# Performance work log

Hardware: AMD Instinct MI355X
Metric: run time of the kernel (lower is better)

Reference implementation:

```python
import jax, jax.numpy as jnp
import numpy as np

OUT_F, IN_F, GROUP = 4096, 4096, 64  # meta['shape'] = (OUT_F, IN_F), group_size=64, axis=1
TOKENS = 8192  # batch*seq flattened


def dequant(W_q, scale, zero):
    # unpack_4bit_u8: high nibble = first half of rows, low nibble = second half
    hi = (W_q >> 4).astype(jnp.float32)
    lo = (W_q & 0xF).astype(jnp.float32)
    W_r = jnp.concatenate([hi, lo], axis=0)      # [G, GROUP]
    W_r = (W_r - zero) * scale                   # group-wise dequant (axis=1 grouping)
    return W_r.reshape(OUT_F, IN_F)


def setup_inputs() -> dict:
    key = jax.random.key(0)
    k0, k1, k2, k3, k4 = jax.random.split(key, 5)
    G = OUT_F * IN_F // GROUP  # 262144 groups
    x = jax.random.normal(k0, (TOKENS, IN_F), dtype=jnp.float32)
    W_q = jax.random.randint(k1, (G // 2, GROUP), 0, 256, dtype=jnp.int32)  # packed bytes
    scale = jax.random.uniform(k2, (G, 1), dtype=jnp.float32) * 0.01 + 1e-4  # 1/scale from quantizer
    zero = jax.random.uniform(k3, (G, 1), dtype=jnp.float32) * 15.0
    bias = jax.random.normal(k4, (OUT_F,), dtype=jnp.float32)
    return {"x": x, "W_q": W_q, "scale": scale, "zero": zero, "bias": bias}


def reference(x, W_q, scale, zero, bias):
    # HQQMatmulNoCacheDeq.forward: out = x @ dequantize().T + bias
    W_r = dequant(W_q, scale, zero)              # [OUT_F, IN_F]
    return x @ W_r.T + bias                      # [TOKENS, OUT_F]
```

## Files before the change

### kernel.cpp

```cpp
#include <hip/hip_runtime.h>
#include <stdint.h>


typedef __attribute__((ext_vector_type(8))) _Float16 half8;
typedef __attribute__((ext_vector_type(4))) float f32x4;

#define M_DIM 8192
#define N_DIM 4096
#define K_DIM 4096

__device__ __forceinline__ void async16(const void* g, void* l) {
  __builtin_amdgcn_global_load_lds(
      (const __attribute__((address_space(1))) void*)g,
      (__attribute__((address_space(3))) void*)l,
      16, 0, 0);
}

__global__ __launch_bounds__(256) void prep(
    const float* __restrict__ x, const int* __restrict__ Wq,
    const float* __restrict__ scale, const float* __restrict__ zero,
    _Float16* __restrict__ xh, _Float16* __restrict__ wh) {
  const int b = blockIdx.x;
  if (b < 16384) {
    const size_t i = ((size_t)b * 256 + threadIdx.x) * 8;
    f32x4 a = *(const f32x4*)(x + i);
    f32x4 c = *(const f32x4*)(x + i + 4);
    half8 h;
    h[0] = (_Float16)a[0]; h[1] = (_Float16)a[1];
    h[2] = (_Float16)a[2]; h[3] = (_Float16)a[3];
    h[4] = (_Float16)c[0]; h[5] = (_Float16)c[1];
    h[6] = (_Float16)c[2]; h[7] = (_Float16)c[3];
    *(half8*)(xh + i) = h;
  } else {
    const int idx = (b - 16384) * 256 + threadIdx.x;
    const int o  = idx >> 9;
    const int kb = (idx & 511) << 3;
    const int g  = (o << 6) + (kb >> 6);
    const int j  = kb & 63;
    const bool hi = (o < 2048);
    const int* src = Wq + (size_t)(hi ? g : g - 131072) * 64 + j;
    const int4 v0 = *(const int4*)src;
    const int4 v1 = *(const int4*)(src + 4);
    const float s  = scale[g];
    const float nz = -zero[g] * s;
    int raw[8] = {v0.x, v0.y, v0.z, v0.w, v1.x, v1.y, v1.z, v1.w};
    half8 h;
#pragma unroll
    for (int r = 0; r < 8; ++r) {
      const int nib = hi ? ((raw[r] >> 4) & 0xF) : (raw[r] & 0xF);
      h[r] = (_Float16)((float)nib * s + nz);
    }
    *(half8*)(wh + (size_t)o * K_DIM + kb) = h;
  }
}

__global__ __launch_bounds__(512, 2) void gemm_f16_deep(
    const _Float16* __restrict__ A, const _Float16* __restrict__ B,
    const float* __restrict__ bias, float* __restrict__ C) {
  __shared__ _Float16 As[3 * 8192];
  __shared__ _Float16 Bs[3 * 8192];

  const int tid  = threadIdx.x;
  const int wave = tid >> 6;
  const int lane = tid & 63;
  const int quad = lane >> 4;
  const int l16  = lane & 15;
  const int wm   = wave >> 2;
  const int wn   = wave & 3;

  const int bid = blockIdx.x;
  const int swb = (bid & 7) * 64 + (bid >> 3);
  const int m0 = (swb >> 4) * 256;
  const int n0 = (swb & 15) * 256;

  const int srow = tid >> 2;
  const int sg   = (((tid & 3) ^ ((srow >> 1) & 3)) << 3);
  const _Float16* gA0 = A + (size_t)(m0 + srow) * K_DIM + sg;
  const _Float16* gA1 = gA0 + (size_t)128 * K_DIM;
  const _Float16* gB0 = B + (size_t)(n0 + srow) * K_DIM + sg;
  const _Float16* gB1 = gB0 + (size_t)128 * K_DIM;
  const int wst = wave * 512;

  const int fro  = ((quad ^ ((l16 >> 1) & 3)) << 3);
  const int arow = wm * 128 + l16;
  const int brow = wn * 64 + l16;

  f32x4 acc[8][4] = {};

  int sR = 0, sN = 8192, sW = 16384;

  async16(gA0,      As + sR + wst);
  async16(gA1,      As + sR + 4096 + wst);
  async16(gB0,      Bs + sR + wst);
  async16(gB1,      Bs + sR + 4096 + wst);
  async16(gA0 + 32, As + sN + wst);
  async16(gA1 + 32, As + sN + 4096 + wst);
  async16(gB0 + 32, Bs + sN + wst);
  async16(gB1 + 32, Bs + sN + 4096 + wst);
  asm volatile("s_waitcnt vmcnt(4)" ::: "memory");
  __builtin_amdgcn_s_barrier();

  const int NT = K_DIM / 32;
#pragma unroll 1
  for (int T = 0; T < NT; ++T) {
    if (T + 2 < NT) {
      const int kk = (T + 2) * 32;
      async16(gA0 + kk, As + sW + wst);
      async16(gA1 + kk, As + sW + 4096 + wst);
      async16(gB0 + kk, Bs + sW + wst);
      async16(gB1 + kk, Bs + sW + 4096 + wst);
    }

    const _Float16* Ab = As + sR;
    const _Float16* Bb = Bs + sR;
    half8 aF[4], bF[4];
#pragma unroll
    for (int j = 0; j < 4; ++j)
      bF[j] = *(const half8*)(Bb + (brow + j * 16) * 32 + fro);
#pragma unroll
    for (int i = 0; i < 4; ++i)
      aF[i] = *(const half8*)(Ab + (arow + i * 16) * 32 + fro);

    __builtin_amdgcn_s_setprio(1);
#pragma unroll
    for (int i = 0; i < 4; ++i)
#pragma unroll
      for (int j = 0; j < 4; ++j)
        acc[i][j] = __builtin_amdgcn_mfma_f32_16x16x32_f16(aF[i], bF[j],
                                                           acc[i][j], 0, 0, 0);
    __builtin_amdgcn_s_setprio(0);

#pragma unroll
    for (int i = 0; i < 4; ++i)
      aF[i] = *(const half8*)(Ab + (arow + 64 + i * 16) * 32 + fro);

    __builtin_amdgcn_s_setprio(1);
#pragma unroll
    for (int i = 0; i < 4; ++i)
#pragma unroll
      for (int j = 0; j < 4; ++j)
        acc[i + 4][j] = __builtin_amdgcn_mfma_f32_16x16x32_f16(aF[i], bF[j],
                                                               acc[i + 4][j],
                                                               0, 0, 0);
    __builtin_amdgcn_s_setprio(0);

    if (T + 2 < NT) {
      asm volatile("s_waitcnt vmcnt(4)" ::: "memory");
      __builtin_amdgcn_s_barrier();
    } else if (T + 1 < NT) {
      asm volatile("s_waitcnt vmcnt(0)" ::: "memory");
      __builtin_amdgcn_s_barrier();
    }
    const int t = sR; sR = sN; sN = sW; sW = t;
  }

#pragma unroll
  for (int j = 0; j < 4; ++j) {
    const int n = n0 + wn * 64 + j * 16 + l16;
    const float bv = bias[n];
#pragma unroll
    for (int i = 0; i < 8; ++i) {
      const int m = m0 + wm * 128 + i * 16 + quad * 4;
      float* p = C + (size_t)m * N_DIM + n;
      f32x4 v = acc[i][j];
      p[0 * N_DIM] = v[0] + bv;
      p[1 * N_DIM] = v[1] + bv;
      p[2 * N_DIM] = v[2] + bv;
      p[3 * N_DIM] = v[3] + bv;
    }
  }
}

__global__ __launch_bounds__(256) void gemm_fp32_fallback(
    const float* __restrict__ x, const int* __restrict__ Wq,
    const float* __restrict__ scale, const float* __restrict__ zero,
    const float* __restrict__ bias, float* __restrict__ C) {
  __shared__ float As[64][16];
  __shared__ float Bs[64][16];
  const int tid = threadIdx.x;
  const int m0 = blockIdx.y * 64;
  const int n0 = blockIdx.x * 64;
  const int tx = tid & 15;
  const int ty = tid >> 4;
  const int lr = tid >> 2;
  const int lc = (tid & 3) << 2;

  float acc[4][4] = {};

  for (int k0 = 0; k0 < K_DIM; k0 += 16) {
    __syncthreads();
    *(f32x4*)&As[lr][lc] = *(const f32x4*)(x + (size_t)(m0 + lr) * K_DIM + k0 + lc);
    {
      const int o = n0 + lr;
      const int k = k0 + lc;
      const int g = (o << 6) + (k >> 6);
      const bool hi = (o < 2048);
      const int* src = Wq + (size_t)(hi ? g : g - 131072) * 64 + (k & 63);
      const int4 v = *(const int4*)src;
      const float s = scale[g];
      const float nz = -zero[g] * s;
      f32x4 b;
      if (hi) {
        b[0] = (float)((v.x >> 4) & 0xF) * s + nz;
        b[1] = (float)((v.y >> 4) & 0xF) * s + nz;
        b[2] = (float)((v.z >> 4) & 0xF) * s + nz;
        b[3] = (float)((v.w >> 4) & 0xF) * s + nz;
      } else {
        b[0] = (float)(v.x & 0xF) * s + nz;
        b[1] = (float)(v.y & 0xF) * s + nz;
        b[2] = (float)(v.z & 0xF) * s + nz;
        b[3] = (float)(v.w & 0xF) * s + nz;
      }
      *(f32x4*)&Bs[lr][lc] = b;
    }
    __syncthreads();
#pragma unroll
    for (int kk = 0; kk < 16; ++kk) {
      float a[4], b[4];
#pragma unroll
      for (int r = 0; r < 4; ++r) a[r] = As[ty * 4 + r][kk];
#pragma unroll
      for (int c = 0; c < 4; ++c) b[c] = Bs[tx * 4 + c][kk];
#pragma unroll
      for (int r = 0; r < 4; ++r)
#pragma unroll
        for (int c = 0; c < 4; ++c) acc[r][c] += a[r] * b[c];
    }
  }
#pragma unroll
  for (int r = 0; r < 4; ++r)
#pragma unroll
    for (int c = 0; c < 4; ++c) {
      const int n = n0 + tx * 4 + c;
      C[(size_t)(m0 + ty * 4 + r) * N_DIM + n] = acc[r][c] + bias[n];
    }
}

extern "C" void kernel_launch(void* const* d_in, const int* in_sizes, int n_in,
                              void* d_out, int out_size, void* d_ws, size_t ws_size,
                              hipStream_t stream) {
  const float* x     = (const float*)d_in[0];
  const int*   Wq    = (const int*)d_in[1];
  const float* scale = (const float*)d_in[2];
  const float* zero  = (const float*)d_in[3];
  const float* bias  = (const float*)d_in[4];
  float* out = (float*)d_out;

  const size_t xh_bytes = (size_t)M_DIM * K_DIM * 2;
  const size_t wh_bytes = (size_t)N_DIM * K_DIM * 2;

  if (ws_size >= xh_bytes + wh_bytes) {
    _Float16* xh = (_Float16*)d_ws;
    _Float16* wh = (_Float16*)((char*)d_ws + xh_bytes);
    prep<<<16384 + 8192, 256, 0, stream>>>(x, Wq, scale, zero, xh, wh);
    gemm_f16_deep<<<(M_DIM / 256) * (N_DIM / 256), 512, 0, stream>>>(xh, wh, bias, out);
  } else {
    dim3 grid(N_DIM / 64, M_DIM / 64);
    gemm_fp32_fallback<<<grid, 256, 0, stream>>>(x, Wq, scale, zero, bias, out);
  }
}
```

Measured before the change: 591.0 us.

## Split GEMM k-step into barrier-fenced halves and unroll the triple-buffer rotation

Restructures the main loop of the f16 GEMM. Each k-step is split into two halves, and the global-to-LDS prefetch of A and B is spread across those halves. Barriers and explicit lgkmcnt waits are placed around each MFMA cluster to get a finer, ping-pong-style interleave of LDS reads, global loads and matrix math. The loop is unrolled by three so the triple-buffer offsets become compile-time constants instead of rotating registers. The intent is better overlap of memory and compute and less address arithmetic, at the cost of four barriers per k-step instead of one, which may add stalls.

```diff
diff --git a/kernel.cpp b/kernel.cpp
--- a/kernel.cpp
+++ b/kernel.cpp
@@ -54,7 +54,7 @@
   }
 }
 
-__global__ __launch_bounds__(512, 2) void gemm_f16_deep(
+__global__ __launch_bounds__(512, 2) void gemm_f16_fine(
     const _Float16* __restrict__ A, const _Float16* __restrict__ B,
     const float* __restrict__ bias, float* __restrict__ C) {
   __shared__ _Float16 As[3 * 8192];
@@ -74,7 +74,7 @@
   const int n0 = (swb & 15) * 256;
 
   const int srow = tid >> 2;
-  const int sg   = (((tid & 3) ^ ((srow >> 1) & 3)) << 3);
+  const int sg   = (((tid & 3) ^ ((tid >> 3) & 3)) << 3);
   const _Float16* gA0 = A + (size_t)(m0 + srow) * K_DIM + sg;
   const _Float16* gA1 = gA0 + (size_t)128 * K_DIM;
   const _Float16* gB0 = B + (size_t)(n0 + srow) * K_DIM + sg;
@@ -87,72 +87,71 @@
 
   f32x4 acc[8][4] = {};
 
-  int sR = 0, sN = 8192, sW = 16384;
-
-  async16(gA0,      As + sR + wst);
-  async16(gA1,      As + sR + 4096 + wst);
-  async16(gB0,      Bs + sR + wst);
-  async16(gB1,      Bs + sR + 4096 + wst);
-  async16(gA0 + 32, As + sN + wst);
-  async16(gA1 + 32, As + sN + 4096 + wst);
-  async16(gB0 + 32, Bs + sN + wst);
-  async16(gB1 + 32, Bs + sN + 4096 + wst);
+  const int NT = K_DIM / 32;
+
+  async16(gA0,      As + wst);
+  async16(gA1,      As + 4096 + wst);
+  async16(gB0,      Bs + wst);
+  async16(gB1,      Bs + 4096 + wst);
+  async16(gA0 + 32, As + 8192 + wst);
+  async16(gA1 + 32, As + 8192 + 4096 + wst);
+  async16(gB0 + 32, Bs + 8192 + wst);
+  async16(gB1 + 32, Bs + 8192 + 4096 + wst);
   asm volatile("s_waitcnt vmcnt(4)" ::: "memory");
   __builtin_amdgcn_s_barrier();
 
-  const int NT = K_DIM / 32;
-#pragma unroll 1
-  for (int T = 0; T < NT; ++T) {
-    if (T + 2 < NT) {
-      const int kk = (T + 2) * 32;
-      async16(gA0 + kk, As + sW + wst);
-      async16(gA1 + kk, As + sW + 4096 + wst);
-      async16(gB0 + kk, Bs + sW + wst);
-      async16(gB1 + kk, Bs + sW + 4096 + wst);
-    }
-
-    const _Float16* Ab = As + sR;
-    const _Float16* Bb = Bs + sR;
-    half8 aF[4], bF[4];
-#pragma unroll
-    for (int j = 0; j < 4; ++j)
-      bF[j] = *(const half8*)(Bb + (brow + j * 16) * 32 + fro);
-#pragma unroll
-    for (int i = 0; i < 4; ++i)
-      aF[i] = *(const half8*)(Ab + (arow + i * 16) * 32 + fro);
-
-    __builtin_amdgcn_s_setprio(1);
-#pragma unroll
-    for (int i = 0; i < 4; ++i)
-#pragma unroll
-      for (int j = 0; j < 4; ++j)
-        acc[i][j] = __builtin_amdgcn_mfma_f32_16x16x32_f16(aF[i], bF[j],
-                                                           acc[i][j], 0, 0, 0);
-    __builtin_amdgcn_s_setprio(0);
-
-#pragma unroll
-    for (int i = 0; i < 4; ++i)
-      aF[i] = *(const half8*)(Ab + (arow + 64 + i * 16) * 32 + fro);
-
-    __builtin_amdgcn_s_setprio(1);
-#pragma unroll
-    for (int i = 0; i < 4; ++i)
-#pragma unroll
-      for (int j = 0; j < 4; ++j)
-        acc[i + 4][j] = __builtin_amdgcn_mfma_f32_16x16x32_f16(aF[i], bF[j],
-                                                               acc[i + 4][j],
-                                                               0, 0, 0);
-    __builtin_amdgcn_s_setprio(0);
-
-    if (T + 2 < NT) {
-      asm volatile("s_waitcnt vmcnt(4)" ::: "memory");
-      __builtin_amdgcn_s_barrier();
-    } else if (T + 1 < NT) {
-      asm volatile("s_waitcnt vmcnt(0)" ::: "memory");
-      __builtin_amdgcn_s_barrier();
-    }
-    const int t = sR; sR = sN; sN = sW; sW = t;
-  }
+#define KSTEP(SR, SW, T)                                                     \
+  {                                                                          \
+    half8 aF[4], bF[4];                                                      \
+                     \
+    _Pragma("unroll") for (int j = 0; j < 4; ++j)                            \
+      bF[j] = *(const half8*)(Bs + (SR) + (brow + j * 16) * 32 + fro);       \
+    _Pragma("unroll") for (int i = 0; i < 4; ++i)                            \
+      aF[i] = *(const half8*)(As + (SR) + (arow + i * 16) * 32 + fro);       \
+    if ((T) + 2 < NT) {                                                      \
+      const int kk = ((T) + 2) * 32;                                         \
+      async16(gA0 + kk, As + (SW) + wst);                                    \
+      async16(gA1 + kk, As + (SW) + 4096 + wst);                             \
+    }                                                                        \
+    __builtin_amdgcn_s_barrier();                                            \
+    asm volatile("s_waitcnt lgkmcnt(0)" ::: "memory");                       \
+    __builtin_amdgcn_s_setprio(1);                                           \
+    _Pragma("unroll") for (int i = 0; i < 4; ++i)                            \
+      _Pragma("unroll") for (int j = 0; j < 4; ++j)                          \
+        acc[i][j] = __builtin_amdgcn_mfma_f32_16x16x32_f16(                  \
+            aF[i], bF[j], acc[i][j], 0, 0, 0);                               \
+    __builtin_amdgcn_s_setprio(0);                                           \
+    __builtin_amdgcn_s_barrier();                                            \
+          \
+    _Pragma("unroll") for (int i = 0; i < 4; ++i)                            \
+      aF[i] = *(const half8*)(As + (SR) + (arow + 64 + i * 16) * 32 + fro);  \
+    if ((T) + 2 < NT) {                                                      \
+      const int kk = ((T) + 2) * 32;                                         \
+      async16(gB0 + kk, Bs + (SW) + wst);                                    \
+      async16(gB1 + kk, Bs + (SW) + 4096 + wst);                             \
+      asm volatile("s_waitcnt vmcnt(4)" ::: "memory");                       \
+    } else {                                                                 \
+      asm volatile("s_waitcnt vmcnt(0)" ::: "memory");                       \
+    }                                                                        \
+    __builtin_amdgcn_s_barrier();                                            \
+    asm volatile("s_waitcnt lgkmcnt(0)" ::: "memory");                       \
+    __builtin_amdgcn_s_setprio(1);                                           \
+    _Pragma("unroll") for (int i = 0; i < 4; ++i)                            \
+      _Pragma("unroll") for (int j = 0; j < 4; ++j)                          \
+        acc[i + 4][j] = __builtin_amdgcn_mfma_f32_16x16x32_f16(              \
+            aF[i], bF[j], acc[i + 4][j], 0, 0, 0);                           \
+    __builtin_amdgcn_s_setprio(0);                                           \
+    __builtin_amdgcn_s_barrier();                                            \
+  }
+
+  for (int T = 0; T < 126; T += 3) {
+    KSTEP(0,     16384, T)
+    KSTEP(8192,  0,     T + 1)
+    KSTEP(16384, 8192,  T + 2)
+  }
+  KSTEP(0,    16384, 126)
+  KSTEP(8192, 0,     127)
+#undef KSTEP
 
 #pragma unroll
   for (int j = 0; j < 4; ++j) {
@@ -253,7 +252,7 @@
     _Float16* xh = (_Float16*)d_ws;
     _Float16* wh = (_Float16*)((char*)d_ws + xh_bytes);
     prep<<<16384 + 8192, 256, 0, stream>>>(x, Wq, scale, zero, xh, wh);
-    gemm_f16_deep<<<(M_DIM / 256) * (N_DIM / 256), 512, 0, stream>>>(xh, wh, bias, out);
+    gemm_f16_fine<<<(M_DIM / 256) * (N_DIM / 256), 512, 0, stream>>>(xh, wh, bias, out);
   } else {
     dim3 grid(N_DIM / 64, M_DIM / 64);
     gemm_fp32_fallback<<<grid, 256, 0, stream>>>(x, Wq, scale, zero, bias, out);
```

Result: faster. 517.3 us (-12.5%).
